# Optimization experiments

Hardware: AMD Instinct MI355X
Metric: run time of the kernel (lower is better)

The kernel has to match this reference:

```python
import jax, jax.numpy as jnp
import numpy as np

N_T = 50000   # target cells
N_S = 100000  # source cells
E = 400000    # nonzeros per sparse operator
IN_CH = 128
OUT_CH = 256
N_MLP = 3     # Linear+ReLU layers per branch (1 + mlp_hidden)


def setup_inputs() -> dict:
    key = jax.random.key(0)
    ks = jax.random.split(key, 20)
    s_in = (2.0 / (IN_CH + OUT_CH)) ** 0.5
    s_hid = (2.0 / (OUT_CH + OUT_CH)) ** 0.5
    s_m = (2.0 / (2 * OUT_CH + OUT_CH)) ** 0.5
    return {
        "x_target": jax.random.normal(ks[0], (N_T, OUT_CH), jnp.float32),
        "x_src0": jax.random.normal(ks[1], (N_S, IN_CH), jnp.float32),
        "x_src1": jax.random.normal(ks[2], (N_S, IN_CH), jnp.float32),
        "vals0": jax.random.normal(ks[3], (E,), jnp.float32),
        "vals1": jax.random.normal(ks[4], (E,), jnp.float32),
        "rows0": jax.random.randint(ks[5], (E,), 0, N_T, jnp.int32),
        "cols0": jax.random.randint(ks[6], (E,), 0, N_S, jnp.int32),
        "rows1": jax.random.randint(ks[7], (E,), 0, N_T, jnp.int32),
        "cols1": jax.random.randint(ks[8], (E,), 0, N_S, jnp.int32),
        "W0": jax.random.normal(ks[9], (IN_CH, OUT_CH), jnp.float32) * s_in,
        "W1": jax.random.normal(ks[10], (IN_CH, OUT_CH), jnp.float32) * s_in,
        "mlp_W0": jax.random.normal(ks[11], (N_MLP, OUT_CH, OUT_CH), jnp.float32) * s_hid,
        "mlp_b0": jnp.zeros((N_MLP, OUT_CH), jnp.float32),
        "mlp_W1": jax.random.normal(ks[12], (N_MLP, OUT_CH, OUT_CH), jnp.float32) * s_hid,
        "mlp_b1": jnp.zeros((N_MLP, OUT_CH), jnp.float32),
        "Wm": jax.random.normal(ks[13], (2 * OUT_CH, OUT_CH), jnp.float32) * s_m,
        "bm": jnp.zeros((OUT_CH,), jnp.float32),
    }


def _branch(x_target, x_src, rows, cols, vals, W, mlp_W, mlp_b, epsilon=0.0):
    # support = x_source @ weight  (channel dims differ)
    support = x_src @ W                                   # [N_S, OUT]
    # propagate: sparse A @ support via gather + segment_sum (signed values kept)
    msgs = vals[:, None] * support[cols]                  # [E, OUT]
    agg = jax.ops.segment_sum(msgs, rows, num_segments=x_target.shape[0])
    h = agg + (1.0 + epsilon) * x_target                  # epsilon residual
    for i in range(N_MLP):                                # Linear -> ReLU, x3
        h = jax.nn.relu(h @ mlp_W[i] + mlp_b[i])
    return h


def reference(x_target, x_src0, x_src1, vals0, vals1, rows0, cols0, rows1, cols1,
              W0, W1, mlp_W0, mlp_b0, mlp_W1, mlp_b1, Wm, bm):
    h0 = _branch(x_target, x_src0, rows0, cols0, vals0, W0, mlp_W0, mlp_b0)
    h1 = _branch(x_target, x_src1, rows1, cols1, vals1, W1, mlp_W1, mlp_b1)
    # merge_type == 'conc': concat along channels then Linear
    return jnp.concatenate([h0, h1], axis=1) @ Wm + bm
```

## Files before the change

kernel.cpp:

```cpp
#include <hip/hip_runtime.h>
#include <stdint.h>

#define NT 50000
#define NS 100000
#define NE 400000
#define CIN 128
#define COUT 256
#define HL 264

typedef unsigned short u16;
typedef short bf8 __attribute__((ext_vector_type(8)));
typedef float f4 __attribute__((ext_vector_type(4)));

__device__ __forceinline__ float bf2f(u16 u) {
  union { unsigned int i; float f; } x; x.i = ((unsigned int)u) << 16; return x.f;
}
__device__ __forceinline__ u16 f2bf(float f) {
  union { float f; unsigned int i; } x; x.f = f;
  return (u16)((x.i + 0x7fffu + ((x.i >> 16) & 1u)) >> 16);
}
__device__ __forceinline__ float loadf(const void* base, size_t eoff, int f32) {
  if (f32) return ((const float*)base)[eoff];
  return bf2f(((const u16*)base)[eoff]);
}

struct DetectArgs { const unsigned int* p[13]; int nw[13]; };

__global__ void detect_all(DetectArgs a, int* __restrict__ flags) {
  __shared__ int s_sane, s_nz;
  const int bi = blockIdx.x;
  const unsigned int* buf = a.p[bi];
  const int nw = a.nw[bi];
  if (threadIdx.x == 0) { s_sane = 0; s_nz = 0; }
  __syncthreads();
  int sane = 0, nz = 0;
  for (int i = threadIdx.x; i < nw; i += 256) {
    unsigned int w = buf[i];
    if (w != 0u) {
      ++nz;
      unsigned int e = (w >> 23) & 0xFFu;
      if (e >= 100u && e <= 140u) ++sane;
    }
  }
  atomicAdd(&s_sane, sane);
  atomicAdd(&s_nz, nz);
  __syncthreads();
  if (threadIdx.x == 0) flags[bi] = (s_nz > 0 && 2 * s_sane > s_nz) ? 1 : 0;
}

__global__ void convert_bf16(const void* __restrict__ src, const int* __restrict__ flag,
                             u16* __restrict__ dst, int n) {
  int t = (blockIdx.x * 256 + threadIdx.x) * 4;
  if (t >= n) return;
  if (*flag) {
    const float* s = (const float*)src + t;
    ushort4 o;
    o.x = f2bf(s[0]); o.y = f2bf(s[1]); o.z = f2bf(s[2]); o.w = f2bf(s[3]);
    *(ushort4*)&dst[t] = o;
  } else {
    *(ushort4*)&dst[t] = *(const ushort4*)((const u16*)src + t);
  }
}

__global__ void transpose_w(const void* __restrict__ src, const int* __restrict__ flag,
                            u16* __restrict__ dst, int K, int N, int total) {
  int t = blockIdx.x * 256 + threadIdx.x;
  if (t >= total) return;
  int f32 = *flag;
  int kn = K * N;
  int mat = t / kn, i = t - mat * kn;
  int n = i / K, k = i - n * K;
  size_t s = (size_t)mat * kn + (size_t)k * N + n;
  dst[t] = f32 ? f2bf(((const float*)src)[s]) : ((const u16*)src)[s];
}

__global__ __launch_bounds__(256, 2)
void fused_mlp(const u16* __restrict__ agg0, const u16* __restrict__ agg1,
               const u16* __restrict__ W0t, const u16* __restrict__ W1t,
               const u16* __restrict__ mW0t, const u16* __restrict__ mW1t,
               const u16* __restrict__ mbc,
               const u16* __restrict__ Wmt,
               const u16* __restrict__ bmc,
               const void* __restrict__ xt, const int* __restrict__ xtflag,
               void* __restrict__ out, const int* __restrict__ outflag, int M) {
  __shared__ __align__(16) u16 sX[64 * HL];
  __shared__ __align__(16) u16 sY[64 * HL];

  const int tid  = threadIdx.x;
  const int wave = tid >> 6;
  const int lane = tid & 63;
  const int m0   = blockIdx.x * 64;
  const int wn   = wave * 64;
  const int mrow = lane & 15;
  const int krow = (lane >> 4) * 8;
  const int erow = (lane >> 4) * 4;
  const int ecol = lane & 15;

  const int xf = *xtflag;

  f4 acc[4][4];

  auto mm_lds = [&](const u16* src, const u16* Bt, int ldb, int bcol0, int K) {
#pragma unroll
    for (int i = 0; i < 4; ++i)
#pragma unroll
      for (int j = 0; j < 4; ++j) acc[i][j] = (f4){0.f, 0.f, 0.f, 0.f};
    const u16* bp[4];
#pragma unroll
    for (int j = 0; j < 4; ++j)
      bp[j] = Bt + (size_t)(wn + j * 16 + mrow) * ldb + bcol0 + krow;
    bf8 bv0[4], bv1[4];
#pragma unroll
    for (int j = 0; j < 4; ++j) bv0[j] = *(const bf8*)(bp[j]);
    for (int k0 = 0; k0 < K; k0 += 32) {
      const int kn = k0 + 32;
      if (kn < K) {
#pragma unroll
        for (int j = 0; j < 4; ++j) bv1[j] = *(const bf8*)(bp[j] + kn);
      }
      bf8 aF[4];
#pragma unroll
      for (int i = 0; i < 4; ++i)
        aF[i] = *(const bf8*)&src[(i * 16 + mrow) * HL + k0 + krow];
#pragma unroll
      for (int i = 0; i < 4; ++i)
#pragma unroll
        for (int j = 0; j < 4; ++j)
          acc[i][j] = __builtin_amdgcn_mfma_f32_16x16x32_bf16(aF[i], bv0[j], acc[i][j], 0, 0, 0);
      if (kn < K) {
#pragma unroll
        for (int j = 0; j < 4; ++j) bv0[j] = bv1[j];
      }
    }
  };

  auto mm_glb = [&](const u16* A, int lda, const u16* Bt, int ldb, int K) {
#pragma unroll
    for (int i = 0; i < 4; ++i)
#pragma unroll
      for (int j = 0; j < 4; ++j) acc[i][j] = (f4){0.f, 0.f, 0.f, 0.f};
    const u16* ap[4];
    const u16* bp[4];
#pragma unroll
    for (int i = 0; i < 4; ++i) {
      int r = m0 + i * 16 + mrow;
      if (r >= M) r = M - 1;
      ap[i] = A + (size_t)r * lda + krow;
    }
#pragma unroll
    for (int j = 0; j < 4; ++j)
      bp[j] = Bt + (size_t)(wn + j * 16 + mrow) * ldb + krow;
    bf8 a0[4], b0[4], a1[4], b1[4];
#pragma unroll
    for (int i = 0; i < 4; ++i) a0[i] = *(const bf8*)(ap[i]);
#pragma unroll
    for (int j = 0; j < 4; ++j) b0[j] = *(const bf8*)(bp[j]);
    for (int k0 = 0; k0 < K; k0 += 32) {
      const int kn = k0 + 32;
      if (kn < K) {
#pragma unroll
        for (int i = 0; i < 4; ++i) a1[i] = *(const bf8*)(ap[i] + kn);
#pragma unroll
        for (int j = 0; j < 4; ++j) b1[j] = *(const bf8*)(bp[j] + kn);
      }
#pragma unroll
      for (int i = 0; i < 4; ++i)
#pragma unroll
        for (int j = 0; j < 4; ++j)
          acc[i][j] = __builtin_amdgcn_mfma_f32_16x16x32_bf16(a0[i], b0[j], acc[i][j], 0, 0, 0);
      if (kn < K) {
#pragma unroll
        for (int i = 0; i < 4; ++i) a0[i] = a1[i];
#pragma unroll
        for (int j = 0; j < 4; ++j) b0[j] = b1[j];
      }
    }
  };

  auto epi_lds = [&](u16* dst, const u16* bias, int relu, int addxt) {
#pragma unroll
    for (int j = 0; j < 4; ++j) {
      const int col = wn + ecol + j * 16;
      const float bv = bias ? bf2f(bias[col]) : 0.f;
#pragma unroll
      for (int i = 0; i < 4; ++i)
#pragma unroll
        for (int r = 0; r < 4; ++r) {
          const int row = erow + i * 16 + r;
          float v = acc[i][j][r] + bv;
          if (addxt) {
            int rr = m0 + row; if (rr >= M) rr = M - 1;
            v += loadf(xt, (size_t)rr * COUT + col, xf);
          }
          if (relu) v = fmaxf(v, 0.f);
          dst[row * HL + col] = f2bf(v);
        }
    }
  };

  mm_glb(agg0, CIN, W0t, CIN, CIN);
  epi_lds(sY, nullptr, 0, 1);  __syncthreads();
  mm_lds(sY, mW0t,                 COUT, 0, COUT);
  epi_lds(sX, mbc + 0 * COUT, 1, 0); __syncthreads();
  mm_lds(sX, mW0t + COUT * COUT,   COUT, 0, COUT);
  epi_lds(sY, mbc + 1 * COUT, 1, 0); __syncthreads();
  mm_lds(sY, mW0t + 2 * COUT * COUT, COUT, 0, COUT);
  epi_lds(sX, mbc + 2 * COUT, 1, 0); __syncthreads();

  mm_lds(sX, Wmt, 512, 0, COUT);
  f4 accP[4][4];
#pragma unroll
  for (int i = 0; i < 4; ++i)
#pragma unroll
    for (int j = 0; j < 4; ++j) accP[i][j] = acc[i][j];

  mm_glb(agg1, CIN, W1t, CIN, CIN);
  epi_lds(sY, nullptr, 0, 1);  __syncthreads();
  mm_lds(sY, mW1t,                 COUT, 0, COUT);
  epi_lds(sX, mbc + 3 * COUT, 1, 0); __syncthreads();
  mm_lds(sX, mW1t + COUT * COUT,   COUT, 0, COUT);
  epi_lds(sY, mbc + 4 * COUT, 1, 0); __syncthreads();
  mm_lds(sY, mW1t + 2 * COUT * COUT, COUT, 0, COUT);
  epi_lds(sX, mbc + 5 * COUT, 1, 0); __syncthreads();

  mm_lds(sX, Wmt, 512, COUT, COUT);

  const int of = *outflag;
#pragma unroll
  for (int j = 0; j < 4; ++j) {
    const int col = wn + ecol + j * 16;
    const float bv = bf2f(bmc[col]);
#pragma unroll
    for (int i = 0; i < 4; ++i)
#pragma unroll
      for (int r = 0; r < 4; ++r) {
        const int rr = m0 + erow + i * 16 + r;
        if (rr < M) {
          const size_t idx = (size_t)rr * COUT + col;
          float v = acc[i][j][r] + accP[i][j][r] + bv;
          if (of) ((float*)out)[idx] = v;
          else    ((u16*)out)[idx] = f2bf(v);
        }
      }
  }
}

__global__ void hist_kernel(const int* __restrict__ rows0, const int* __restrict__ rows1,
                            int* __restrict__ cnt) {
  int t = blockIdx.x * 256 + threadIdx.x;
  if (t >= 2 * NE) return;
  int seg = (t < NE) ? rows0[t] : (NT + rows1[t - NE]);
  atomicAdd(&cnt[seg], 1);
}

__global__ void scanA(const int* __restrict__ cnt, int* __restrict__ incl,
                      int* __restrict__ bsum, int n) {
  __shared__ int sd[256];
  int t = threadIdx.x, g = blockIdx.x * 256 + t;
  int v = (g < n) ? cnt[g] : 0;
  sd[t] = v; __syncthreads();
  for (int o = 1; o < 256; o <<= 1) {
    int x = (t >= o) ? sd[t - o] : 0;
    __syncthreads();
    sd[t] += x;
    __syncthreads();
  }
  if (g < n) incl[g] = sd[t];
  if (t == 255) bsum[blockIdx.x] = sd[255];
}

__global__ void scanB(int* __restrict__ bsum, int nb) {
  __shared__ int sd[512];
  int t = threadIdx.x;
  int v = (t < nb) ? bsum[t] : 0;
  sd[t] = v; __syncthreads();
  for (int o = 1; o < 512; o <<= 1) {
    int x = (t >= o) ? sd[t - o] : 0;
    __syncthreads();
    sd[t] += x;
    __syncthreads();
  }
  if (t < nb) bsum[t] = sd[t] - v;
}

__global__ void scanC(const int* __restrict__ cnt, const int* __restrict__ incl,
                      const int* __restrict__ bsum, int* __restrict__ row_ptr,
                      int n, int total) {
  int g = blockIdx.x * 256 + threadIdx.x;
  if (g == 0) row_ptr[n] = total;
  if (g >= n) return;
  row_ptr[g] = incl[g] - cnt[g] + bsum[blockIdx.x];
}

__global__ void scatter_kernel(const int* __restrict__ rows0, const int* __restrict__ cols0,
                               const void* __restrict__ vals0, const int* __restrict__ v0f,
                               const int* __restrict__ rows1, const int* __restrict__ cols1,
                               const void* __restrict__ vals1, const int* __restrict__ v1f,
                               const int* __restrict__ row_ptr, int* __restrict__ cnt,
                               int* __restrict__ scol, float* __restrict__ sval) {
  int t = blockIdx.x * 256 + threadIdx.x;
  if (t >= 2 * NE) return;
  int seg, col; float v;
  if (t < NE) { seg = rows0[t]; col = cols0[t]; v = loadf(vals0, t, *v0f); }
  else { int e = t - NE; seg = NT + rows1[e]; col = cols1[e]; v = loadf(vals1, e, *v1f); }
  int pos = row_ptr[seg] + atomicAdd(&cnt[seg], 1);
  scol[pos] = col;
  sval[pos] = v;
}

__global__ __launch_bounds__(256)
void spmm_gather(const int* __restrict__ row_ptr, const int* __restrict__ scol,
                 const float* __restrict__ sval, const u16* __restrict__ Xs,
                 u16* __restrict__ agg, int seg_base) {
  int wid = blockIdx.x * 4 + (threadIdx.x >> 6);
  int lane = threadIdx.x & 63;
  if (wid >= NT) return;
  int seg = seg_base + wid;
  int p0 = row_ptr[seg], p1 = row_ptr[seg + 1];
  int c = lane * 2;
  float a0 = 0.f, a1 = 0.f;
  int p = p0;
  for (; p + 3 < p1; p += 4) {
    int c0 = scol[p], c1 = scol[p + 1], c2 = scol[p + 2], c3 = scol[p + 3];
    float v0 = sval[p], v1 = sval[p + 1], v2 = sval[p + 2], v3 = sval[p + 3];
    ushort2 s0 = *(const ushort2*)&Xs[(size_t)c0 * CIN + c];
    ushort2 s1 = *(const ushort2*)&Xs[(size_t)c1 * CIN + c];
    ushort2 s2 = *(const ushort2*)&Xs[(size_t)c2 * CIN + c];
    ushort2 s3 = *(const ushort2*)&Xs[(size_t)c3 * CIN + c];
    a0 += v0 * bf2f(s0.x); a1 += v0 * bf2f(s0.y);
    a0 += v1 * bf2f(s1.x); a1 += v1 * bf2f(s1.y);
    a0 += v2 * bf2f(s2.x); a1 += v2 * bf2f(s2.y);
    a0 += v3 * bf2f(s3.x); a1 += v3 * bf2f(s3.y);
  }
  for (; p < p1; ++p) {
    int cc = scol[p];
    float v = sval[p];
    ushort2 s = *(const ushort2*)&Xs[(size_t)cc * CIN + c];
    a0 += v * bf2f(s.x); a1 += v * bf2f(s.y);
  }
  ushort2 o;
  o.x = f2bf(a0); o.y = f2bf(a1);
  *(ushort2*)&agg[(size_t)wid * CIN + c] = o;
}

extern "C" void kernel_launch(void* const* d_in, const int* in_sizes, int n_in,
                              void* d_out, int out_size, void* d_ws, size_t ws_size,
                              hipStream_t stream) {
  (void)n_in; (void)out_size; (void)ws_size;

  int I_xt, I_xs0, I_xs1, I_v0, I_v1, I_r0, I_c0, I_r1, I_c1,
      I_W0, I_W1, I_mW0, I_mb0, I_mW1, I_mb1, I_Wm, I_bm;
  if (in_sizes[0] == 32768) {
    I_W0 = 0; I_W1 = 1; I_Wm = 2; I_bm = 3; I_c0 = 4; I_c1 = 5;
    I_mW0 = 6; I_mW1 = 7; I_mb0 = 8; I_mb1 = 9; I_r0 = 10; I_r1 = 11;
    I_v0 = 12; I_v1 = 13; I_xs0 = 14; I_xs1 = 15; I_xt = 16;
  } else {
    I_xt = 0; I_xs0 = 1; I_xs1 = 2; I_v0 = 3; I_v1 = 4; I_r0 = 5; I_c0 = 6;
    I_r1 = 7; I_c1 = 8; I_W0 = 9; I_W1 = 10; I_mW0 = 11; I_mb0 = 12;
    I_mW1 = 13; I_mb1 = 14; I_Wm = 15; I_bm = 16;
  }
  const void* x_target = d_in[I_xt];
  const void* x_src0   = d_in[I_xs0];
  const void* x_src1   = d_in[I_xs1];
  const void* vals0    = d_in[I_v0];
  const void* vals1    = d_in[I_v1];
  const int* rows0     = (const int*)d_in[I_r0];
  const int* cols0     = (const int*)d_in[I_c0];
  const int* rows1     = (const int*)d_in[I_r1];
  const int* cols1     = (const int*)d_in[I_c1];
  const void* W0       = d_in[I_W0];
  const void* W1       = d_in[I_W1];
  const void* mW0      = d_in[I_mW0];
  const void* mb0      = d_in[I_mb0];
  const void* mW1      = d_in[I_mW1];
  const void* mb1      = d_in[I_mb1];
  const void* Wm       = d_in[I_Wm];
  const void* bm       = d_in[I_bm];

  char* ws = (char*)d_ws;
  size_t off = 0;
  auto alloc = [&](size_t bytes) -> char* {
    off = (off + 255) & ~(size_t)255;
    char* p = ws + off;
    off += bytes;
    return p;
  };
  int* flags = (int*)alloc(16 * 4);
  u16* W0t   = (u16*)alloc((size_t)COUT * CIN * 2);
  u16* W1t   = (u16*)alloc((size_t)COUT * CIN * 2);
  u16* mW0t  = (u16*)alloc((size_t)3 * COUT * COUT * 2);
  u16* mW1t  = (u16*)alloc((size_t)3 * COUT * COUT * 2);
  u16* Wmt   = (u16*)alloc((size_t)COUT * 512 * 2);
  u16* mbc   = (u16*)alloc((size_t)2 * 3 * COUT * 2);
  u16* bmc   = (u16*)alloc((size_t)COUT * 2);
  u16* xsc   = (u16*)alloc((size_t)NS * CIN * 2);
  u16* agg0  = (u16*)alloc((size_t)NT * CIN * 2);
  u16* agg1  = (u16*)alloc((size_t)NT * CIN * 2);
  int* cnt     = (int*)alloc((size_t)2 * NT * 4);
  int* row_ptr = (int*)alloc(((size_t)2 * NT + 1) * 4);
  int* incl    = (int*)alloc((size_t)2 * NT * 4);
  int* bsum    = (int*)alloc(512 * 4);
  int* scol    = (int*)alloc((size_t)2 * NE * 4);
  float* sval  = (float*)alloc((size_t)2 * NE * 4);

  DetectArgs da;
  const void* dp[13]  = {x_target, x_src0, x_src1, vals0, vals1, W0, W1,
                         mW0, mb0, mW1, mb1, Wm, bm};
  const int   dn[13]  = {NT * COUT, NS * CIN, NS * CIN, NE, NE,
                         CIN * COUT, CIN * COUT, 3 * COUT * COUT, 3 * COUT,
                         3 * COUT * COUT, 3 * COUT, 512 * COUT, COUT};
  for (int i = 0; i < 13; ++i) {
    da.p[i] = (const unsigned int*)dp[i];
    int nw = dn[i] / 2; if (nw > 8192) nw = 8192; if (nw < 1) nw = 1;
    da.nw[i] = nw;
  }
  detect_all<<<13, 256, 0, stream>>>(da, flags);

  transpose_w<<<(CIN * COUT + 255) / 256, 256, 0, stream>>>(W0, flags + 5, W0t, CIN, COUT, CIN * COUT);
  transpose_w<<<(CIN * COUT + 255) / 256, 256, 0, stream>>>(W1, flags + 6, W1t, CIN, COUT, CIN * COUT);
  transpose_w<<<(3 * COUT * COUT + 255) / 256, 256, 0, stream>>>(mW0, flags + 7, mW0t, COUT, COUT, 3 * COUT * COUT);
  transpose_w<<<(3 * COUT * COUT + 255) / 256, 256, 0, stream>>>(mW1, flags + 9, mW1t, COUT, COUT, 3 * COUT * COUT);
  transpose_w<<<(512 * COUT + 255) / 256, 256, 0, stream>>>(Wm, flags + 11, Wmt, 512, COUT, 512 * COUT);
  convert_bf16<<<1, 256, 0, stream>>>(mb0, flags + 8,  mbc,            3 * COUT);
  convert_bf16<<<1, 256, 0, stream>>>(mb1, flags + 10, mbc + 3 * COUT, 3 * COUT);
  convert_bf16<<<1, 256, 0, stream>>>(bm,  flags + 12, bmc,            COUT);

  hipMemsetAsync(cnt, 0, (size_t)2 * NT * 4, stream);
  hist_kernel<<<(2 * NE + 255) / 256, 256, 0, stream>>>(rows0, rows1, cnt);
  const int nseg = 2 * NT;
  const int nb = (nseg + 255) / 256;
  scanA<<<nb, 256, 0, stream>>>(cnt, incl, bsum, nseg);
  scanB<<<1, 512, 0, stream>>>(bsum, nb);
  scanC<<<nb, 256, 0, stream>>>(cnt, incl, bsum, row_ptr, nseg, 2 * NE);
  hipMemsetAsync(cnt, 0, (size_t)2 * NT * 4, stream);
  scatter_kernel<<<(2 * NE + 255) / 256, 256, 0, stream>>>(
      rows0, cols0, vals0, flags + 3, rows1, cols1, vals1, flags + 4,
      row_ptr, cnt, scol, sval);

  convert_bf16<<<(NS * CIN / 4 + 255) / 256, 256, 0, stream>>>(x_src0, flags + 1, xsc, NS * CIN);
  spmm_gather<<<NT / 4, 256, 0, stream>>>(row_ptr, scol, sval, xsc, agg0, 0);
  convert_bf16<<<(NS * CIN / 4 + 255) / 256, 256, 0, stream>>>(x_src1, flags + 2, xsc, NS * CIN);
  spmm_gather<<<NT / 4, 256, 0, stream>>>(row_ptr, scol, sval, xsc, agg1, NT);

  fused_mlp<<<(NT + 63) / 64, 256, 0, stream>>>(
      agg0, agg1, W0t, W1t, mW0t, mW1t, mbc, Wmt, bmc,
      x_target, flags + 0, d_out, flags + 0, NT);
}
```

Measured before the change: 645.3 us.

## Shrink MLP row tile, fuse prep kernels, gather directly from fp32 sources

The fused MLP kernel now processes 32 rows per block instead of 64, with a 2x4 accumulator tile and launch bounds raised to 4 blocks per CU. The goal is lower register and LDS pressure and more blocks in flight. The cost is that each block re-reads the full weight matrices for half as many rows, so weight traffic through the caches doubles. The small weight and bias conversion launches are merged into one prep kernel, and the counter memsets are folded into detect_all and scanC. spmm_gather now reads the fp32 source features directly, which removes the two bf16 conversion passes but makes each gather fetch twice as many bytes.

```diff
diff --git a/kernel.cpp b/kernel.cpp
--- a/kernel.cpp
+++ b/kernel.cpp
@@ -7,6 +7,7 @@
 #define CIN 128
 #define COUT 256
 #define HL 264
+#define SROW 32
 
 typedef unsigned short u16;
 typedef short bf8 __attribute__((ext_vector_type(8)));
@@ -26,9 +27,14 @@
 
 struct DetectArgs { const unsigned int* p[13]; int nw[13]; };
 
-__global__ void detect_all(DetectArgs a, int* __restrict__ flags) {
+__global__ void detect_all(DetectArgs a, int* __restrict__ flags, int* __restrict__ cnt) {
+  const int bi = blockIdx.x;
+  if (bi >= 13) {
+    int t = ((bi - 13) * 256 + threadIdx.x) * 4;
+    if (t < 2 * NT) *(int4*)&cnt[t] = (int4){0, 0, 0, 0};
+    return;
+  }
   __shared__ int s_sane, s_nz;
-  const int bi = blockIdx.x;
   const unsigned int* buf = a.p[bi];
   const int nw = a.nw[bi];
   if (threadIdx.x == 0) { s_sane = 0; s_nz = 0; }
@@ -48,33 +54,96 @@
   if (threadIdx.x == 0) flags[bi] = (s_nz > 0 && 2 * s_sane > s_nz) ? 1 : 0;
 }
 
-__global__ void convert_bf16(const void* __restrict__ src, const int* __restrict__ flag,
-                             u16* __restrict__ dst, int n) {
-  int t = (blockIdx.x * 256 + threadIdx.x) * 4;
-  if (t >= n) return;
-  if (*flag) {
-    const float* s = (const float*)src + t;
-    ushort4 o;
-    o.x = f2bf(s[0]); o.y = f2bf(s[1]); o.z = f2bf(s[2]); o.w = f2bf(s[3]);
-    *(ushort4*)&dst[t] = o;
+struct PrepArgs {
+  const void* src[8];
+  u16* dst[8];
+  int flagidx[8];
+  int K[8], N[8], mode[8];
+  int cum[9];
+};
+
+__global__ void prep_all(PrepArgs a, const int* __restrict__ flags) {
+  int t = blockIdx.x * 256 + threadIdx.x;
+  if (t >= a.cum[8]) return;
+  int r = 0;
+#pragma unroll
+  for (int q = 0; q < 7; ++q)
+    if (t >= a.cum[q + 1]) r = q + 1;
+  int i = t - a.cum[r];
+  int f32 = flags[a.flagidx[r]];
+  if (a.mode[r]) {
+    int K = a.K[r], N = a.N[r], kn = K * N;
+    int mat = i / kn, ii = i - mat * kn;
+    int n = ii / K, k = ii - n * K;
+    size_t s = (size_t)mat * kn + (size_t)k * N + n;
+    a.dst[r][i] = f32 ? f2bf(((const float*)a.src[r])[s]) : ((const u16*)a.src[r])[s];
   } else {
-    *(ushort4*)&dst[t] = *(const ushort4*)((const u16*)src + t);
-  }
-}
-
-__global__ void transpose_w(const void* __restrict__ src, const int* __restrict__ flag,
-                            u16* __restrict__ dst, int K, int N, int total) {
-  int t = blockIdx.x * 256 + threadIdx.x;
-  if (t >= total) return;
-  int f32 = *flag;
-  int kn = K * N;
-  int mat = t / kn, i = t - mat * kn;
-  int n = i / K, k = i - n * K;
-  size_t s = (size_t)mat * kn + (size_t)k * N + n;
-  dst[t] = f32 ? f2bf(((const float*)src)[s]) : ((const u16*)src)[s];
-}
-
-__global__ __launch_bounds__(256, 2)
+    a.dst[r][i] = f32 ? f2bf(((const float*)a.src[r])[i]) : ((const u16*)a.src[r])[i];
+  }
+}
+
+template <int K, int LDB>
+__device__ __forceinline__ void mm_ldsA(f4 (&acc)[2][4], const u16* __restrict__ src,
+                                        const u16* __restrict__ Bt, int wn, int bcol0,
+                                        int mrow, int krow) {
+#pragma unroll
+  for (int i = 0; i < 2; ++i)
+#pragma unroll
+    for (int j = 0; j < 4; ++j) acc[i][j] = (f4){0.f, 0.f, 0.f, 0.f};
+  const u16* bp[4];
+#pragma unroll
+  for (int j = 0; j < 4; ++j)
+    bp[j] = Bt + (size_t)(wn + j * 16 + mrow) * LDB + bcol0 + krow;
+  const u16* ap = src + mrow * HL + krow;
+#pragma unroll
+  for (int k0 = 0; k0 < K; k0 += 32) {
+    bf8 aF[2], bF[4];
+#pragma unroll
+    for (int i = 0; i < 2; ++i) aF[i] = *(const bf8*)(ap + i * 16 * HL + k0);
+#pragma unroll
+    for (int j = 0; j < 4; ++j) bF[j] = *(const bf8*)(bp[j] + k0);
+#pragma unroll
+    for (int i = 0; i < 2; ++i)
+#pragma unroll
+      for (int j = 0; j < 4; ++j)
+        acc[i][j] = __builtin_amdgcn_mfma_f32_16x16x32_bf16(aF[i], bF[j], acc[i][j], 0, 0, 0);
+  }
+}
+
+__device__ __forceinline__ void mm_glbA(f4 (&acc)[2][4], const u16* __restrict__ A,
+                                        int m0, int M, const u16* __restrict__ Bt,
+                                        int wn, int mrow, int krow) {
+#pragma unroll
+  for (int i = 0; i < 2; ++i)
+#pragma unroll
+    for (int j = 0; j < 4; ++j) acc[i][j] = (f4){0.f, 0.f, 0.f, 0.f};
+  const u16* ap[2];
+#pragma unroll
+  for (int i = 0; i < 2; ++i) {
+    int r = m0 + i * 16 + mrow;
+    if (r >= M) r = M - 1;
+    ap[i] = A + (size_t)r * CIN + krow;
+  }
+  const u16* bp[4];
+#pragma unroll
+  for (int j = 0; j < 4; ++j)
+    bp[j] = Bt + (size_t)(wn + j * 16 + mrow) * CIN + krow;
+#pragma unroll
+  for (int k0 = 0; k0 < CIN; k0 += 32) {
+    bf8 aF[2], bF[4];
+#pragma unroll
+    for (int i = 0; i < 2; ++i) aF[i] = *(const bf8*)(ap[i] + k0);
+#pragma unroll
+    for (int j = 0; j < 4; ++j) bF[j] = *(const bf8*)(bp[j] + k0);
+#pragma unroll
+    for (int i = 0; i < 2; ++i)
+#pragma unroll
+      for (int j = 0; j < 4; ++j)
+        acc[i][j] = __builtin_amdgcn_mfma_f32_16x16x32_bf16(aF[i], bF[j], acc[i][j], 0, 0, 0);
+  }
+}
+
+__global__ __launch_bounds__(256, 4)
 void fused_mlp(const u16* __restrict__ agg0, const u16* __restrict__ agg1,
                const u16* __restrict__ W0t, const u16* __restrict__ W1t,
                const u16* __restrict__ mW0t, const u16* __restrict__ mW1t,
@@ -83,13 +152,13 @@
                const u16* __restrict__ bmc,
                const void* __restrict__ xt, const int* __restrict__ xtflag,
                void* __restrict__ out, const int* __restrict__ outflag, int M) {
-  __shared__ __align__(16) u16 sX[64 * HL];
-  __shared__ __align__(16) u16 sY[64 * HL];
+  __shared__ __align__(16) u16 sX[SROW * HL];
+  __shared__ __align__(16) u16 sY[SROW * HL];
 
   const int tid  = threadIdx.x;
   const int wave = tid >> 6;
   const int lane = tid & 63;
-  const int m0   = blockIdx.x * 64;
+  const int m0   = blockIdx.x * SROW;
   const int wn   = wave * 64;
   const int mrow = lane & 15;
   const int krow = (lane >> 4) * 8;
@@ -98,92 +167,15 @@
 
   const int xf = *xtflag;
 
-  f4 acc[4][4];
-
-  auto mm_lds = [&](const u16* src, const u16* Bt, int ldb, int bcol0, int K) {
-#pragma unroll
-    for (int i = 0; i < 4; ++i)
-#pragma unroll
-      for (int j = 0; j < 4; ++j) acc[i][j] = (f4){0.f, 0.f, 0.f, 0.f};
-    const u16* bp[4];
-#pragma unroll
-    for (int j = 0; j < 4; ++j)
-      bp[j] = Bt + (size_t)(wn + j * 16 + mrow) * ldb + bcol0 + krow;
-    bf8 bv0[4], bv1[4];
-#pragma unroll
-    for (int j = 0; j < 4; ++j) bv0[j] = *(const bf8*)(bp[j]);
-    for (int k0 = 0; k0 < K; k0 += 32) {
-      const int kn = k0 + 32;
-      if (kn < K) {
-#pragma unroll
-        for (int j = 0; j < 4; ++j) bv1[j] = *(const bf8*)(bp[j] + kn);
-      }
-      bf8 aF[4];
-#pragma unroll
-      for (int i = 0; i < 4; ++i)
-        aF[i] = *(const bf8*)&src[(i * 16 + mrow) * HL + k0 + krow];
-#pragma unroll
-      for (int i = 0; i < 4; ++i)
-#pragma unroll
-        for (int j = 0; j < 4; ++j)
-          acc[i][j] = __builtin_amdgcn_mfma_f32_16x16x32_bf16(aF[i], bv0[j], acc[i][j], 0, 0, 0);
-      if (kn < K) {
-#pragma unroll
-        for (int j = 0; j < 4; ++j) bv0[j] = bv1[j];
-      }
-    }
-  };
-
-  auto mm_glb = [&](const u16* A, int lda, const u16* Bt, int ldb, int K) {
-#pragma unroll
-    for (int i = 0; i < 4; ++i)
-#pragma unroll
-      for (int j = 0; j < 4; ++j) acc[i][j] = (f4){0.f, 0.f, 0.f, 0.f};
-    const u16* ap[4];
-    const u16* bp[4];
-#pragma unroll
-    for (int i = 0; i < 4; ++i) {
-      int r = m0 + i * 16 + mrow;
-      if (r >= M) r = M - 1;
-      ap[i] = A + (size_t)r * lda + krow;
-    }
-#pragma unroll
-    for (int j = 0; j < 4; ++j)
-      bp[j] = Bt + (size_t)(wn + j * 16 + mrow) * ldb + krow;
-    bf8 a0[4], b0[4], a1[4], b1[4];
-#pragma unroll
-    for (int i = 0; i < 4; ++i) a0[i] = *(const bf8*)(ap[i]);
-#pragma unroll
-    for (int j = 0; j < 4; ++j) b0[j] = *(const bf8*)(bp[j]);
-    for (int k0 = 0; k0 < K; k0 += 32) {
-      const int kn = k0 + 32;
-      if (kn < K) {
-#pragma unroll
-        for (int i = 0; i < 4; ++i) a1[i] = *(const bf8*)(ap[i] + kn);
-#pragma unroll
-        for (int j = 0; j < 4; ++j) b1[j] = *(const bf8*)(bp[j] + kn);
-      }
-#pragma unroll
-      for (int i = 0; i < 4; ++i)
-#pragma unroll
-        for (int j = 0; j < 4; ++j)
-          acc[i][j] = __builtin_amdgcn_mfma_f32_16x16x32_bf16(a0[i], b0[j], acc[i][j], 0, 0, 0);
-      if (kn < K) {
-#pragma unroll
-        for (int i = 0; i < 4; ++i) a0[i] = a1[i];
-#pragma unroll
-        for (int j = 0; j < 4; ++j) b0[j] = b1[j];
-      }
-    }
-  };
-
-  auto epi_lds = [&](u16* dst, const u16* bias, int relu, int addxt) {
+  f4 acc[2][4];
+
+  auto epi = [&](u16* dst, const u16* bias, int relu, int addxt) {
 #pragma unroll
     for (int j = 0; j < 4; ++j) {
       const int col = wn + ecol + j * 16;
       const float bv = bias ? bf2f(bias[col]) : 0.f;
 #pragma unroll
-      for (int i = 0; i < 4; ++i)
+      for (int i = 0; i < 2; ++i)
 #pragma unroll
         for (int r = 0; r < 4; ++r) {
           const int row = erow + i * 16 + r;
@@ -198,32 +190,32 @@
     }
   };
 
-  mm_glb(agg0, CIN, W0t, CIN, CIN);
-  epi_lds(sY, nullptr, 0, 1);  __syncthreads();
-  mm_lds(sY, mW0t,                 COUT, 0, COUT);
-  epi_lds(sX, mbc + 0 * COUT, 1, 0); __syncthreads();
-  mm_lds(sX, mW0t + COUT * COUT,   COUT, 0, COUT);
-  epi_lds(sY, mbc + 1 * COUT, 1, 0); __syncthreads();
-  mm_lds(sY, mW0t + 2 * COUT * COUT, COUT, 0, COUT);
-  epi_lds(sX, mbc + 2 * COUT, 1, 0); __syncthreads();
-
-  mm_lds(sX, Wmt, 512, 0, COUT);
-  f4 accP[4][4];
-#pragma unroll
-  for (int i = 0; i < 4; ++i)
+  mm_glbA(acc, agg0, m0, M, W0t, wn, mrow, krow);
+  epi(sY, nullptr, 0, 1);  __syncthreads();
+  mm_ldsA<COUT, COUT>(acc, sY, mW0t,                 wn, 0, mrow, krow);
+  epi(sX, mbc + 0 * COUT, 1, 0); __syncthreads();
+  mm_ldsA<COUT, COUT>(acc, sX, mW0t + COUT * COUT,   wn, 0, mrow, krow);
+  epi(sY, mbc + 1 * COUT, 1, 0); __syncthreads();
+  mm_ldsA<COUT, COUT>(acc, sY, mW0t + 2 * COUT * COUT, wn, 0, mrow, krow);
+  epi(sX, mbc + 2 * COUT, 1, 0); __syncthreads();
+
+  mm_ldsA<COUT, 512>(acc, sX, Wmt, wn, 0, mrow, krow);
+  f4 accP[2][4];
+#pragma unroll
+  for (int i = 0; i < 2; ++i)
 #pragma unroll
     for (int j = 0; j < 4; ++j) accP[i][j] = acc[i][j];
 
-  mm_glb(agg1, CIN, W1t, CIN, CIN);
-  epi_lds(sY, nullptr, 0, 1);  __syncthreads();
-  mm_lds(sY, mW1t,                 COUT, 0, COUT);
-  epi_lds(sX, mbc + 3 * COUT, 1, 0); __syncthreads();
-  mm_lds(sX, mW1t + COUT * COUT,   COUT, 0, COUT);
-  epi_lds(sY, mbc + 4 * COUT, 1, 0); __syncthreads();
-  mm_lds(sY, mW1t + 2 * COUT * COUT, COUT, 0, COUT);
-  epi_lds(sX, mbc + 5 * COUT, 1, 0); __syncthreads();
-
-  mm_lds(sX, Wmt, 512, COUT, COUT);
+  mm_glbA(acc, agg1, m0, M, W1t, wn, mrow, krow);
+  epi(sY, nullptr, 0, 1);  __syncthreads();
+  mm_ldsA<COUT, COUT>(acc, sY, mW1t,                 wn, 0, mrow, krow);
+  epi(sX, mbc + 3 * COUT, 1, 0); __syncthreads();
+  mm_ldsA<COUT, COUT>(acc, sX, mW1t + COUT * COUT,   wn, 0, mrow, krow);
+  epi(sY, mbc + 4 * COUT, 1, 0); __syncthreads();
+  mm_ldsA<COUT, COUT>(acc, sY, mW1t + 2 * COUT * COUT, wn, 0, mrow, krow);
+  epi(sX, mbc + 5 * COUT, 1, 0); __syncthreads();
+
+  mm_ldsA<COUT, 512>(acc, sX, Wmt, wn, COUT, mrow, krow);
 
   const int of = *outflag;
 #pragma unroll
@@ -231,7 +223,7 @@
     const int col = wn + ecol + j * 16;
     const float bv = bf2f(bmc[col]);
 #pragma unroll
-    for (int i = 0; i < 4; ++i)
+    for (int i = 0; i < 2; ++i)
 #pragma unroll
       for (int r = 0; r < 4; ++r) {
         const int rr = m0 + erow + i * 16 + r;
@@ -283,13 +275,14 @@
   if (t < nb) bsum[t] = sd[t] - v;
 }
 
-__global__ void scanC(const int* __restrict__ cnt, const int* __restrict__ incl,
+__global__ void scanC(int* __restrict__ cnt, const int* __restrict__ incl,
                       const int* __restrict__ bsum, int* __restrict__ row_ptr,
                       int n, int total) {
   int g = blockIdx.x * 256 + threadIdx.x;
   if (g == 0) row_ptr[n] = total;
   if (g >= n) return;
   row_ptr[g] = incl[g] - cnt[g] + bsum[blockIdx.x];
+  cnt[g] = 0;
 }
 
 __global__ void scatter_kernel(const int* __restrict__ rows0, const int* __restrict__ cols0,
@@ -310,8 +303,8 @@
 
 __global__ __launch_bounds__(256)
 void spmm_gather(const int* __restrict__ row_ptr, const int* __restrict__ scol,
-                 const float* __restrict__ sval, const u16* __restrict__ Xs,
-                 u16* __restrict__ agg, int seg_base) {
+                 const float* __restrict__ sval, const void* __restrict__ Xsrc,
+                 const int* __restrict__ xsflag, u16* __restrict__ agg, int seg_base) {
   int wid = blockIdx.x * 4 + (threadIdx.x >> 6);
   int lane = threadIdx.x & 63;
   if (wid >= NT) return;
@@ -320,23 +313,44 @@
   int c = lane * 2;
   float a0 = 0.f, a1 = 0.f;
   int p = p0;
-  for (; p + 3 < p1; p += 4) {
-    int c0 = scol[p], c1 = scol[p + 1], c2 = scol[p + 2], c3 = scol[p + 3];
-    float v0 = sval[p], v1 = sval[p + 1], v2 = sval[p + 2], v3 = sval[p + 3];
-    ushort2 s0 = *(const ushort2*)&Xs[(size_t)c0 * CIN + c];
-    ushort2 s1 = *(const ushort2*)&Xs[(size_t)c1 * CIN + c];
-    ushort2 s2 = *(const ushort2*)&Xs[(size_t)c2 * CIN + c];
-    ushort2 s3 = *(const ushort2*)&Xs[(size_t)c3 * CIN + c];
-    a0 += v0 * bf2f(s0.x); a1 += v0 * bf2f(s0.y);
-    a0 += v1 * bf2f(s1.x); a1 += v1 * bf2f(s1.y);
-    a0 += v2 * bf2f(s2.x); a1 += v2 * bf2f(s2.y);
-    a0 += v3 * bf2f(s3.x); a1 += v3 * bf2f(s3.y);
-  }
-  for (; p < p1; ++p) {
-    int cc = scol[p];
-    float v = sval[p];
-    ushort2 s = *(const ushort2*)&Xs[(size_t)cc * CIN + c];
-    a0 += v * bf2f(s.x); a1 += v * bf2f(s.y);
+  if (*xsflag) {
+    const float* X = (const float*)Xsrc;
+    for (; p + 3 < p1; p += 4) {
+      int c0 = scol[p], c1 = scol[p + 1], c2 = scol[p + 2], c3 = scol[p + 3];
+      float v0 = sval[p], v1 = sval[p + 1], v2 = sval[p + 2], v3 = sval[p + 3];
+      float2 s0 = *(const float2*)&X[(size_t)c0 * CIN + c];
+      float2 s1 = *(const float2*)&X[(size_t)c1 * CIN + c];
+      float2 s2 = *(const float2*)&X[(size_t)c2 * CIN + c];
+      float2 s3 = *(const float2*)&X[(size_t)c3 * CIN + c];
+      a0 += v0 * s0.x; a1 += v0 * s0.y;
+      a0 += v1 * s1.x; a1 += v1 * s1.y;
+      a0 += v2 * s2.x; a1 += v2 * s2.y;
+      a0 += v3 * s3.x; a1 += v3 * s3.y;
+    }
+    for (; p < p1; ++p) {
+      float v = sval[p];
+      float2 s = *(const float2*)&X[(size_t)scol[p] * CIN + c];
+      a0 += v * s.x; a1 += v * s.y;
+    }
+  } else {
+    const u16* X = (const u16*)Xsrc;
+    for (; p + 3 < p1; p += 4) {
+      int c0 = scol[p], c1 = scol[p + 1], c2 = scol[p + 2], c3 = scol[p + 3];
+      float v0 = sval[p], v1 = sval[p + 1], v2 = sval[p + 2], v3 = sval[p + 3];
+      ushort2 s0 = *(const ushort2*)&X[(size_t)c0 * CIN + c];
+      ushort2 s1 = *(const ushort2*)&X[(size_t)c1 * CIN + c];
+      ushort2 s2 = *(const ushort2*)&X[(size_t)c2 * CIN + c];
+      ushort2 s3 = *(const ushort2*)&X[(size_t)c3 * CIN + c];
+      a0 += v0 * bf2f(s0.x); a1 += v0 * bf2f(s0.y);
+      a0 += v1 * bf2f(s1.x); a1 += v1 * bf2f(s1.y);
+      a0 += v2 * bf2f(s2.x); a1 += v2 * bf2f(s2.y);
+      a0 += v3 * bf2f(s3.x); a1 += v3 * bf2f(s3.y);
+    }
+    for (; p < p1; ++p) {
+      float v = sval[p];
+      ushort2 s = *(const ushort2*)&X[(size_t)scol[p] * CIN + c];
+      a0 += v * bf2f(s.x); a1 += v * bf2f(s.y);
+    }
   }
   ushort2 o;
   o.x = f2bf(a0); o.y = f2bf(a1);
@@ -393,7 +407,6 @@
   u16* Wmt   = (u16*)alloc((size_t)COUT * 512 * 2);
   u16* mbc   = (u16*)alloc((size_t)2 * 3 * COUT * 2);
   u16* bmc   = (u16*)alloc((size_t)COUT * 2);
-  u16* xsc   = (u16*)alloc((size_t)NS * CIN * 2);
   u16* agg0  = (u16*)alloc((size_t)NT * CIN * 2);
   u16* agg1  = (u16*)alloc((size_t)NT * CIN * 2);
   int* cnt     = (int*)alloc((size_t)2 * NT * 4);
@@ -414,35 +427,40 @@
     int nw = dn[i] / 2; if (nw > 8192) nw = 8192; if (nw < 1) nw = 1;
     da.nw[i] = nw;
   }
-  detect_all<<<13, 256, 0, stream>>>(da, flags);
-
-  transpose_w<<<(CIN * COUT + 255) / 256, 256, 0, stream>>>(W0, flags + 5, W0t, CIN, COUT, CIN * COUT);
-  transpose_w<<<(CIN * COUT + 255) / 256, 256, 0, stream>>>(W1, flags + 6, W1t, CIN, COUT, CIN * COUT);
-  transpose_w<<<(3 * COUT * COUT + 255) / 256, 256, 0, stream>>>(mW0, flags + 7, mW0t, COUT, COUT, 3 * COUT * COUT);
-  transpose_w<<<(3 * COUT * COUT + 255) / 256, 256, 0, stream>>>(mW1, flags + 9, mW1t, COUT, COUT, 3 * COUT * COUT);
-  transpose_w<<<(512 * COUT + 255) / 256, 256, 0, stream>>>(Wm, flags + 11, Wmt, 512, COUT, 512 * COUT);
-  convert_bf16<<<1, 256, 0, stream>>>(mb0, flags + 8,  mbc,            3 * COUT);
-  convert_bf16<<<1, 256, 0, stream>>>(mb1, flags + 10, mbc + 3 * COUT, 3 * COUT);
-  convert_bf16<<<1, 256, 0, stream>>>(bm,  flags + 12, bmc,            COUT);
-
-  hipMemsetAsync(cnt, 0, (size_t)2 * NT * 4, stream);
+  const int zb = (2 * NT + 1023) / 1024;
+  detect_all<<<13 + zb, 256, 0, stream>>>(da, flags, cnt);
+
+  PrepArgs pa;
+  const void* psrc[8] = {W0, W1, mW0, mW1, Wm, mb0, mb1, bm};
+  u16* pdst[8]        = {W0t, W1t, mW0t, mW1t, Wmt, mbc, mbc + 3 * COUT, bmc};
+  const int pflag[8]  = {5, 6, 7, 9, 11, 8, 10, 12};
+  const int pK[8]     = {CIN, CIN, COUT, COUT, 512, 0, 0, 0};
+  const int pN[8]     = {COUT, COUT, COUT, COUT, COUT, 0, 0, 0};
+  const int pmode[8]  = {1, 1, 1, 1, 1, 0, 0, 0};
+  const int ptot[8]   = {CIN * COUT, CIN * COUT, 3 * COUT * COUT, 3 * COUT * COUT,
+                         512 * COUT, 3 * COUT, 3 * COUT, COUT};
+  pa.cum[0] = 0;
+  for (int i = 0; i < 8; ++i) {
+    pa.src[i] = psrc[i]; pa.dst[i] = pdst[i]; pa.flagidx[i] = pflag[i];
+    pa.K[i] = pK[i]; pa.N[i] = pN[i]; pa.mode[i] = pmode[i];
+    pa.cum[i + 1] = pa.cum[i] + ptot[i];
+  }
+  prep_all<<<(pa.cum[8] + 255) / 256, 256, 0, stream>>>(pa, flags);
+
   hist_kernel<<<(2 * NE + 255) / 256, 256, 0, stream>>>(rows0, rows1, cnt);
   const int nseg = 2 * NT;
   const int nb = (nseg + 255) / 256;
   scanA<<<nb, 256, 0, stream>>>(cnt, incl, bsum, nseg);
   scanB<<<1, 512, 0, stream>>>(bsum, nb);
   scanC<<<nb, 256, 0, stream>>>(cnt, incl, bsum, row_ptr, nseg, 2 * NE);
-  hipMemsetAsync(cnt, 0, (size_t)2 * NT * 4, stream);
   scatter_kernel<<<(2 * NE + 255) / 256, 256, 0, stream>>>(
       rows0, cols0, vals0, flags + 3, rows1, cols1, vals1, flags + 4,
       row_ptr, cnt, scol, sval);
 
-  convert_bf16<<<(NS * CIN / 4 + 255) / 256, 256, 0, stream>>>(x_src0, flags + 1, xsc, NS * CIN);
-  spmm_gather<<<NT / 4, 256, 0, stream>>>(row_ptr, scol, sval, xsc, agg0, 0);
-  convert_bf16<<<(NS * CIN / 4 + 255) / 256, 256, 0, stream>>>(x_src1, flags + 2, xsc, NS * CIN);
-  spmm_gather<<<NT / 4, 256, 0, stream>>>(row_ptr, scol, sval, xsc, agg1, NT);
-
-  fused_mlp<<<(NT + 63) / 64, 256, 0, stream>>>(
+  spmm_gather<<<NT / 4, 256, 0, stream>>>(row_ptr, scol, sval, x_src0, flags + 1, agg0, 0);
+  spmm_gather<<<NT / 4, 256, 0, stream>>>(row_ptr, scol, sval, x_src1, flags + 2, agg1, NT);
+
+  fused_mlp<<<(NT + SROW - 1) / SROW, 256, 0, stream>>>(
       agg0, agg1, W0t, W1t, mW0t, mW1t, mbc, Wmt, bmc,
       x_target, flags + 0, d_out, flags + 0, NT);
 }
```

Measured after the change: 668.0 us. 3.5% more time.
